# Kernel tuning notes

Measured on AMD Instinct MI355X. Metric: run time of the kernel, lower is better.

Reference implementation:

```python
import jax, jax.numpy as jnp
import numpy as np

N_NODES = 50000
N_GRAPHS = 64
HIDDEN = 128
INPUT = 128
NEG_SLOPE = 0.2


def _gat_layer(x, src, dst, W, a_src, a_dst, b, n_nodes):
    # x: [N, Fin]; src/dst: [E] (self-loops already included)
    h = x @ W                              # [N, H]
    alpha_s = h @ a_src                    # [N]
    alpha_d = h @ a_dst                    # [N]
    e = alpha_s[src] + alpha_d[dst]        # [E]
    e = jnp.where(e > 0, e, NEG_SLOPE * e)  # leaky_relu(0.2)
    # segment softmax over destination node
    m = jax.ops.segment_max(e, dst, num_segments=n_nodes)  # [N]
    m = jnp.where(jnp.isfinite(m), m, 0.0)
    ee = jnp.exp(e - m[dst])
    s = jax.ops.segment_sum(ee, dst, num_segments=n_nodes)
    coef = ee / (s[dst] + 1e-16)           # [E]
    out = jax.ops.segment_sum(h[src] * coef[:, None], dst, num_segments=n_nodes)
    return out + b


def setup_inputs() -> dict:
    key = jax.random.key(0)
    ks = jax.random.split(key, 16)
    x = jax.random.normal(ks[0], (N_NODES, INPUT), dtype=jnp.float32)
    edge_index = jax.random.randint(ks[1], (2, 600000), 0, N_NODES, dtype=jnp.int64 if jax.config.x64_enabled else jnp.int32).astype(jnp.int32)
    batch = jnp.sort(jax.random.randint(ks[2], (N_NODES,), 0, N_GRAPHS)).astype(jnp.int32)
    def glorot(k, shape):
        lim = float(np.sqrt(6.0 / (shape[0] + shape[-1])))
        return jax.random.uniform(k, shape, jnp.float32, -lim, lim)
    params = {}
    dims = [(INPUT, HIDDEN), (HIDDEN, HIDDEN), (HIDDEN, HIDDEN)]
    for i, (fi, fo) in enumerate(dims, 1):
        params[f"W{i}"] = glorot(ks[3 * i], (fi, fo))
        params[f"a_src{i}"] = glorot(ks[3 * i + 1], (fo,)) * 0.1
        params[f"a_dst{i}"] = glorot(ks[3 * i + 2], (fo,)) * 0.1
        params[f"b{i}"] = jnp.zeros((fo,), jnp.float32)
    return dict(x=x, edge_index=edge_index, batch=batch, **params)


def reference(x, edge_index, batch,
              W1, a_src1, a_dst1, b1,
              W2, a_src2, a_dst2, b2,
              W3, a_src3, a_dst3, b3):
    n = x.shape[0]
    loops = jnp.arange(n, dtype=edge_index.dtype)
    src = jnp.concatenate([edge_index[0], loops])  # PyG add_self_loops=True
    dst = jnp.concatenate([edge_index[1], loops])
    h = jax.nn.elu(_gat_layer(x, src, dst, W1, a_src1, a_dst1, b1, n))
    h = jax.nn.elu(_gat_layer(h, src, dst, W2, a_src2, a_dst2, b2, n))
    h = jax.nn.elu(_gat_layer(h, src, dst, W3, a_src3, a_dst3, b3, n))
    # global_mean_pool
    sums = jax.ops.segment_sum(h, batch, num_segments=N_GRAPHS)
    cnt = jax.ops.segment_sum(jnp.ones((n,), h.dtype), batch, num_segments=N_GRAPHS)
    return sums / jnp.maximum(cnt, 1.0)[:, None]
```

## Files before the change

### kernel.cpp

```cpp
#include <hip/hip_runtime.h>
#include <math.h>

#define N_NODES 50000
#define N_GRAPHS 64
#define HID 128
#define SCAN_B 196
#define NODE_BLKS 196
#define NBUCK 128
#define AP 132

typedef _Float16 half8 __attribute__((ext_vector_type(8)));
typedef float f32x4 __attribute__((ext_vector_type(4)));
typedef int i32x4 __attribute__((ext_vector_type(4)));

__device__ __forceinline__ float lrelu(float e) { return e > 0.f ? e : 0.2f * e; }
__device__ __forceinline__ float elu_fast(float o) { return o > 0.f ? o : __expf(o) - 1.f; }

__device__ __forceinline__ void fmix_lo(float& a, int h2, float c) {
    asm("v_fma_mix_f32 %0, %1, %2, %0 op_sel_hi:[1,0,0]" : "+v"(a) : "v"(h2), "v"(c));
}
__device__ __forceinline__ void fmix_hi(float& a, int h2, float c) {
    asm("v_fma_mix_f32 %0, %1, %2, %0 op_sel:[1,0,0] op_sel_hi:[1,0,0]" : "+v"(a) : "v"(h2), "v"(c));
}

__global__ void count_prep(const int* __restrict__ dst, int n_e, int nblk,
                           int* __restrict__ counts, int* __restrict__ start,
                           int* __restrict__ dhist, int* __restrict__ gcur,
                           const float* __restrict__ W0, const float* __restrict__ W1,
                           const float* __restrict__ W2,
                           const float* __restrict__ as0, const float* __restrict__ ad0,
                           const float* __restrict__ as1, const float* __restrict__ ad1,
                           const float* __restrict__ as2, const float* __restrict__ ad2,
                           _Float16* __restrict__ Wh0, _Float16* __restrict__ Wh1,
                           _Float16* __restrict__ Wh2,
                           float* __restrict__ wfold) {
    int blk = blockIdx.x;
    if (blk < nblk) {
        if (blk == 0) {
            if (threadIdx.x <= N_GRAPHS) start[threadIdx.x] = -1;
            if (threadIdx.x < NBUCK) { dhist[threadIdx.x] = 0; gcur[threadIdx.x] = 0; }
        }
        int e = blk * 256 + threadIdx.x;
        if (e < n_e) atomicAdd(&counts[dst[e]], 1);
        return;
    }
    int b = blk - nblk;
    if (b < 24) {
        int layer = b >> 3;
        const float* W = layer == 0 ? W0 : (layer == 1 ? W1 : W2);
        _Float16* Wh = layer == 0 ? Wh0 : (layer == 1 ? Wh1 : Wh2);
        int t = (b & 7) * 256 + threadIdx.x;
        int lane = t & 63;
        int nt = (t >> 6) & 7;
        int kt = t >> 9;
        int n = nt * 16 + (lane & 15);
        int kbase = kt * 32 + (lane >> 4) * 8;
#pragma unroll
        for (int j = 0; j < 8; ++j) {
            float w = W[(size_t)(kbase + j) * 128 + n];
            Wh[(size_t)t * 8 + j] = (_Float16)w;
        }
    } else {
        int idx = b - 24;
        int layer = idx >> 1, which = idx & 1;
        const float* W = layer == 0 ? W0 : (layer == 1 ? W1 : W2);
        const float* a = which == 0 ? (layer == 0 ? as0 : (layer == 1 ? as1 : as2))
                                    : (layer == 0 ? ad0 : (layer == 1 ? ad1 : ad2));
        int k = threadIdx.x;
        if (k < 128) {
            float s = 0.f;
            for (int j = 0; j < 128; ++j) s = fmaf(W[k * 128 + j], a[j], s);
            wfold[idx * 128 + k] = s;
        }
    }
}

__global__ __launch_bounds__(256) void block_reduce(const int* __restrict__ counts,
                                                    int* __restrict__ bsum) {
    __shared__ int red[256];
    int t = threadIdx.x;
    int i = blockIdx.x * 256 + t;
    red[t] = (i < N_NODES) ? counts[i] : 0;
    __syncthreads();
#pragma unroll
    for (int off = 128; off; off >>= 1) {
        if (t < off) red[t] += red[t + off];
        __syncthreads();
    }
    if (t == 0) bsum[blockIdx.x] = red[0];
}

__global__ __launch_bounds__(256) void block_scan(const int* __restrict__ counts,
                                                  const int* __restrict__ bsum,
                                                  const int* __restrict__ batch,
                                                  int* __restrict__ offs,
                                                  int* __restrict__ cursor,
                                                  int* __restrict__ start,
                                                  int* __restrict__ dhist) {
    __shared__ int sb[256];
    __shared__ int sh[256];
    __shared__ int lh[NBUCK];
    int t = threadIdx.x;
    if (t < NBUCK) lh[t] = 0;
    int v = (t < SCAN_B) ? bsum[t] : 0;
    sb[t] = v;
    __syncthreads();
#pragma unroll
    for (int off = 1; off < 256; off <<= 1) {
        int u = (t >= off) ? sb[t - off] : 0;
        __syncthreads();
        sb[t] += u;
        __syncthreads();
    }
    int bpre = (blockIdx.x == 0) ? 0 : sb[blockIdx.x - 1];
    if (blockIdx.x == 0 && t == SCAN_B - 1) offs[N_NODES] = sb[t];

    int i = blockIdx.x * 256 + t;
    int c = (i < N_NODES) ? counts[i] : 0;
    sh[t] = c;
    __syncthreads();
#pragma unroll
    for (int off = 1; off < 256; off <<= 1) {
        int u = (t >= off) ? sh[t - off] : 0;
        __syncthreads();
        sh[t] += u;
        __syncthreads();
    }
    if (i < N_NODES) {
        int e = bpre + sh[t] - c;
        offs[i] = e;
        cursor[i] = e;
        int b = batch[i];
        if (i == 0) start[b] = 0;
        else if (batch[i - 1] != b) start[b] = i;
        atomicAdd(&lh[c < NBUCK - 1 ? c : NBUCK - 1], 1);
    }
    __syncthreads();
    if (t < NBUCK) {
        int n = lh[t];
        if (n) atomicAdd(&dhist[t], n);
    }
}

__global__ __launch_bounds__(256) void scatter_kernel(const int* __restrict__ src,
                                                      const int* __restrict__ dst, int n_e,
                                                      int* __restrict__ cursor,
                                                      int* __restrict__ csr_src,
                                                      float* __restrict__ outz,
                                                      const int* __restrict__ offs,
                                                      const int* __restrict__ dhist,
                                                      int* __restrict__ gcur,
                                                      int* __restrict__ order) {
    int gid = blockIdx.x * 256 + threadIdx.x;
    if (gid < N_GRAPHS * HID) outz[gid] = 0.f;
    if (gid < n_e) {
        int d = dst[gid];
        int pos = atomicAdd(&cursor[d], 1);
        csr_src[pos] = src[gid];
    }
    if (blockIdx.x >= NODE_BLKS) return;

    __shared__ int lh[NBUCK], sc[NBUCK], lbase[NBUCK];
    int t = threadIdx.x;
    if (t < NBUCK) lh[t] = 0;
    __syncthreads();
    int b = -1, lpos = 0;
    if (gid < N_NODES) {
        int deg = offs[gid + 1] - offs[gid];
        b = deg < NBUCK - 1 ? deg : NBUCK - 1;
        lpos = atomicAdd(&lh[b], 1);
    }
    __syncthreads();
    if (t < NBUCK) sc[t] = dhist[t];
    __syncthreads();
    for (int off = 1; off < NBUCK; off <<= 1) {
        int u = (t < NBUCK && t >= off) ? sc[t - off] : 0;
        __syncthreads();
        if (t < NBUCK) sc[t] += u;
        __syncthreads();
    }
    if (t < NBUCK) {
        int excl = t ? sc[t - 1] : 0;
        int cnt = lh[t];
        int bb = cnt ? atomicAdd(&gcur[t], cnt) : 0;
        lbase[t] = excl + bb;
    }
    __syncthreads();
    if (gid < N_NODES) order[lbase[b] + lpos] = gid;
}

__global__ __launch_bounds__(256) void gemm_mfma(const float* __restrict__ X,
                                                 const _Float16* __restrict__ Wh,
                                                 const float* __restrict__ wsv,
                                                 const float* __restrict__ wdv,
                                                 _Float16* __restrict__ H16,
                                                 float* __restrict__ AS,
                                                 float* __restrict__ AD) {
    __shared__ float wsL[128], wdL[128];
    int t = threadIdx.x;
    if (t < 128) wsL[t] = wsv[t];
    else if (t < 256) wdL[t - 128] = wdv[t - 128];
    __syncthreads();

    int wave = t >> 6, lane = t & 63;
    int m15 = lane & 15, quad = lane >> 4;
    int rowbase = blockIdx.x * 64 + wave * 16;
    int arow = rowbase + m15;
    bool arow_ok = arow < N_NODES;

    f32x4 acc[8];
#pragma unroll
    for (int nt = 0; nt < 8; ++nt) acc[nt] = (f32x4){0.f, 0.f, 0.f, 0.f};
    float as_p = 0.f, ad_p = 0.f;

    const float* xrow = X + (size_t)arow * 128 + quad * 8;
#pragma unroll
    for (int kt = 0; kt < 4; ++kt) {
        f32x4 a0 = (f32x4){0.f, 0.f, 0.f, 0.f};
        f32x4 a1 = (f32x4){0.f, 0.f, 0.f, 0.f};
        if (arow_ok) {
            a0 = *(const f32x4*)(xrow + kt * 32);
            a1 = *(const f32x4*)(xrow + kt * 32 + 4);
        }
        int kb = kt * 32 + quad * 8;
        half8 ah;
#pragma unroll
        for (int j = 0; j < 4; ++j) {
            as_p = fmaf(a0[j], wsL[kb + j], as_p);
            ad_p = fmaf(a0[j], wdL[kb + j], ad_p);
            as_p = fmaf(a1[j], wsL[kb + 4 + j], as_p);
            ad_p = fmaf(a1[j], wdL[kb + 4 + j], ad_p);
            ah[j] = (_Float16)a0[j];
            ah[4 + j] = (_Float16)a1[j];
        }
#pragma unroll
        for (int nt = 0; nt < 8; ++nt) {
            size_t fidx = ((size_t)((kt * 8 + nt) * 64 + lane)) * 8;
            half8 bh = *(const half8*)(Wh + fidx);
            acc[nt] = __builtin_amdgcn_mfma_f32_16x16x32_f16(ah, bh, acc[nt], 0, 0, 0);
        }
    }

#pragma unroll
    for (int nt = 0; nt < 8; ++nt) {
        int c = nt * 16 + m15;
#pragma unroll
        for (int reg = 0; reg < 4; ++reg) {
            int gr = rowbase + quad * 4 + reg;
            if (gr < N_NODES) H16[(size_t)gr * 128 + c] = (_Float16)acc[nt][reg];
        }
    }
    as_p += __shfl_xor(as_p, 16);
    ad_p += __shfl_xor(ad_p, 16);
    as_p += __shfl_xor(as_p, 32);
    ad_p += __shfl_xor(ad_p, 32);
    if (quad == 0 && arow_ok) { AS[arow] = as_p; AD[arow] = ad_p; }
}

__global__ __launch_bounds__(256) void aggregate_kernel(const _Float16* __restrict__ H16,
                                                        const float* __restrict__ AS,
                                                        const float* __restrict__ AD,
                                                        const int* __restrict__ offs,
                                                        const int* __restrict__ csr_src,
                                                        const int* __restrict__ order,
                                                        const float* __restrict__ bias,
                                                        const _Float16* __restrict__ Whn,
                                                        const float* __restrict__ wfn,
                                                        _Float16* __restrict__ Hn,
                                                        float* __restrict__ ASn,
                                                        float* __restrict__ ADn,
                                                        float* __restrict__ OUT) {
    __shared__ int2 sh_sp[16][64];
    __shared__ _Float16 aW[16][AP];
    __shared__ int nds[16];
    int tid = threadIdx.x;
    int quad = tid >> 4;
    int l16 = tid & 15;
    int node = order[blockIdx.x * 16 + quad];

    int beg = offs[node];
    int deg = offs[node + 1] - beg;
    float ad = AD[node];
    float eself = lrelu(AS[node] + ad);
    const i32x4* H4 = (const i32x4*)H16;
    i32x4 hsv = H4[(size_t)node * 16 + l16];
    bool fast = deg <= 64;

    float m, ssum = 0.f, ps;
    if (fast) {
        float mym = -INFINITY;
        for (int i = l16; i < deg; i += 16) {
            int sv = csr_src[beg + i];
            float e = lrelu(AS[sv] + ad);
            sh_sp[quad][i] = make_int2(sv, __float_as_int(e));
            mym = fmaxf(mym, e);
        }
#pragma unroll
        for (int off = 8; off; off >>= 1) mym = fmaxf(mym, __shfl_xor(mym, off, 16));
        m = fmaxf(mym, eself);
        ps = __expf(eself - m);
        for (int i = l16; i < deg; i += 16) {
            int2 sp = sh_sp[quad][i];
            float p = __expf(__int_as_float(sp.y) - m);
            sh_sp[quad][i] = make_int2(sp.x, __float_as_int(p));
            ssum += p;
        }
    } else {
        float mym = -INFINITY;
        for (int i = beg + l16; i < beg + deg; i += 16)
            mym = fmaxf(mym, lrelu(AS[csr_src[i]] + ad));
#pragma unroll
        for (int off = 8; off; off >>= 1) mym = fmaxf(mym, __shfl_xor(mym, off, 16));
        m = fmaxf(mym, eself);
        ps = __expf(eself - m);
        for (int i = beg + l16; i < beg + deg; i += 16)
            ssum += __expf(lrelu(AS[csr_src[i]] + ad) - m);
    }

    float accA[8] = {0.f, 0.f, 0.f, 0.f, 0.f, 0.f, 0.f, 0.f};
    float accB[8] = {0.f, 0.f, 0.f, 0.f, 0.f, 0.f, 0.f, 0.f};

    if (fast) {
        int k = 0;
        for (; k + 3 < deg; k += 4) {
            int2 sp0 = sh_sp[quad][k];
            int2 sp1 = sh_sp[quad][k + 1];
            int2 sp2 = sh_sp[quad][k + 2];
            int2 sp3 = sh_sp[quad][k + 3];
            i32x4 h0 = H4[(size_t)sp0.x * 16 + l16];
            i32x4 h1 = H4[(size_t)sp1.x * 16 + l16];
            i32x4 h2 = H4[(size_t)sp2.x * 16 + l16];
            i32x4 h3 = H4[(size_t)sp3.x * 16 + l16];
            float c0 = __int_as_float(sp0.y), c1 = __int_as_float(sp1.y);
            float c2 = __int_as_float(sp2.y), c3 = __int_as_float(sp3.y);
#pragma unroll
            for (int j = 0; j < 4; ++j) {
                fmix_lo(accA[2 * j], h0[j], c0);
                fmix_hi(accA[2 * j + 1], h0[j], c0);
                fmix_lo(accB[2 * j], h1[j], c1);
                fmix_hi(accB[2 * j + 1], h1[j], c1);
            }
#pragma unroll
            for (int j = 0; j < 4; ++j) {
                fmix_lo(accA[2 * j], h2[j], c2);
                fmix_hi(accA[2 * j + 1], h2[j], c2);
                fmix_lo(accB[2 * j], h3[j], c3);
                fmix_hi(accB[2 * j + 1], h3[j], c3);
            }
        }
        for (; k < deg; ++k) {
            int2 sp0 = sh_sp[quad][k];
            float c0 = __int_as_float(sp0.y);
            i32x4 h0 = H4[(size_t)sp0.x * 16 + l16];
#pragma unroll
            for (int j = 0; j < 4; ++j) {
                fmix_lo(accA[2 * j], h0[j], c0);
                fmix_hi(accA[2 * j + 1], h0[j], c0);
            }
        }
    } else {
        for (int k = 0; k < deg; ++k) {
            int s = csr_src[beg + k];
            float c = __expf(lrelu(AS[s] + ad) - m);
            i32x4 h0 = H4[(size_t)s * 16 + l16];
#pragma unroll
            for (int j = 0; j < 4; ++j) {
                fmix_lo(accA[2 * j], h0[j], c);
                fmix_hi(accA[2 * j + 1], h0[j], c);
            }
        }
    }

#pragma unroll
    for (int j = 0; j < 4; ++j) {
        fmix_lo(accA[2 * j], hsv[j], ps);
        fmix_hi(accA[2 * j + 1], hsv[j], ps);
    }
#pragma unroll
    for (int off = 8; off; off >>= 1) ssum += __shfl_xor(ssum, off, 16);
    float inv = __builtin_amdgcn_rcpf(ssum + ps + 1e-16f);

    int c0i = l16 * 8;
    f32x4 b0 = ((const f32x4*)bias)[l16 * 2];
    f32x4 b1 = ((const f32x4*)bias)[l16 * 2 + 1];
    f32x4 o0, o1;
    o0.x = elu_fast(fmaf(accA[0] + accB[0], inv, b0.x));
    o0.y = elu_fast(fmaf(accA[1] + accB[1], inv, b0.y));
    o0.z = elu_fast(fmaf(accA[2] + accB[2], inv, b0.z));
    o0.w = elu_fast(fmaf(accA[3] + accB[3], inv, b0.w));
    o1.x = elu_fast(fmaf(accA[4] + accB[4], inv, b1.x));
    o1.y = elu_fast(fmaf(accA[5] + accB[5], inv, b1.y));
    o1.z = elu_fast(fmaf(accA[6] + accB[6], inv, b1.z));
    o1.w = elu_fast(fmaf(accA[7] + accB[7], inv, b1.w));
    if (OUT) {
        ((f32x4*)OUT)[(size_t)node * 32 + l16 * 2] = o0;
        ((f32x4*)OUT)[(size_t)node * 32 + l16 * 2 + 1] = o1;
    }

    if (Whn) {
        const float* wsn = wfn;
        const float* wdn = wfn + 128;
        float asn = o0.x * wsn[c0i] + o0.y * wsn[c0i + 1] + o0.z * wsn[c0i + 2] +
                    o0.w * wsn[c0i + 3] + o1.x * wsn[c0i + 4] + o1.y * wsn[c0i + 5] +
                    o1.z * wsn[c0i + 6] + o1.w * wsn[c0i + 7];
        float adn = o0.x * wdn[c0i] + o0.y * wdn[c0i + 1] + o0.z * wdn[c0i + 2] +
                    o0.w * wdn[c0i + 3] + o1.x * wdn[c0i + 4] + o1.y * wdn[c0i + 5] +
                    o1.z * wdn[c0i + 6] + o1.w * wdn[c0i + 7];
#pragma unroll
        for (int off = 8; off; off >>= 1) {
            asn += __shfl_xor(asn, off, 16);
            adn += __shfl_xor(adn, off, 16);
        }
        if (l16 == 0) {
            ASn[node] = asn;
            ADn[node] = adn;
            nds[quad] = node;
        }
        half8 hh;
        hh[0] = (_Float16)o0.x; hh[1] = (_Float16)o0.y;
        hh[2] = (_Float16)o0.z; hh[3] = (_Float16)o0.w;
        hh[4] = (_Float16)o1.x; hh[5] = (_Float16)o1.y;
        hh[6] = (_Float16)o1.z; hh[7] = (_Float16)o1.w;
        *(half8*)&aW[quad][c0i] = hh;
        __syncthreads();

        int wv = tid >> 6, lane = tid & 63;
        int m15 = lane & 15, eq = lane >> 4;
        f32x4 acc0 = (f32x4){0.f, 0.f, 0.f, 0.f};
        f32x4 acc1 = (f32x4){0.f, 0.f, 0.f, 0.f};
#pragma unroll
        for (int kt = 0; kt < 4; ++kt) {
            half8 ah = *(const half8*)&aW[m15][kt * 32 + eq * 8];
            half8 bh0 = *(const half8*)(Whn + ((size_t)((kt * 8 + wv * 2) * 64 + lane)) * 8);
            half8 bh1 = *(const half8*)(Whn + ((size_t)((kt * 8 + wv * 2 + 1) * 64 + lane)) * 8);
            acc0 = __builtin_amdgcn_mfma_f32_16x16x32_f16(ah, bh0, acc0, 0, 0, 0);
            acc1 = __builtin_amdgcn_mfma_f32_16x16x32_f16(ah, bh1, acc1, 0, 0, 0);
        }
#pragma unroll
        for (int reg = 0; reg < 4; ++reg) {
            int nid = nds[eq * 4 + reg];
            Hn[(size_t)nid * 128 + wv * 32 + m15] = (_Float16)acc0[reg];
            Hn[(size_t)nid * 128 + wv * 32 + 16 + m15] = (_Float16)acc1[reg];
        }
    }
}

__device__ __forceinline__ int estart(const int* __restrict__ start, int g) {
    for (; g < N_GRAPHS; ++g) {
        int v = start[g];
        if (v >= 0) return v;
    }
    return N_NODES;
}

__global__ __launch_bounds__(128) void pool_kernel(const float* __restrict__ F,
                                                   const int* __restrict__ start,
                                                   float* __restrict__ out) {
    int b = blockIdx.x;
    int g = b >> 4, sub = b & 15;
    int c = threadIdx.x;
    int s0 = estart(start, g), e0 = estart(start, g + 1);
    float acc = 0.f;
    for (int i = s0 + sub; i < e0; i += 16) acc += F[(size_t)i * 128 + c];
    int cnt = e0 - s0;
    float r = 1.f / (float)(cnt > 1 ? cnt : 1);
    atomicAdd(&out[(size_t)g * 128 + c], acc * r);
}

extern "C" void kernel_launch(void* const* d_in, const int* in_sizes, int n_in,
                              void* d_out, int out_size, void* d_ws, size_t ws_size,
                              hipStream_t stream) {
    const float* x = (const float*)d_in[0];
    const int* edge_index = (const int*)d_in[1];
    const int* batch = (const int*)d_in[2];
    const float* W[3]   = {(const float*)d_in[3], (const float*)d_in[7], (const float*)d_in[11]};
    const float* avs[3] = {(const float*)d_in[4], (const float*)d_in[8], (const float*)d_in[12]};
    const float* avd[3] = {(const float*)d_in[5], (const float*)d_in[9], (const float*)d_in[13]};
    const float* bb[3]  = {(const float*)d_in[6], (const float*)d_in[10], (const float*)d_in[14]};
    int E0 = in_sizes[1] / 2;
    const int* esrc = edge_index;
    const int* edst = edge_index + E0;

    char* p = (char*)d_ws;
    auto alloc = [&](size_t bytes) -> void* {
        void* q = (void*)p;
        p += (bytes + 255) & ~(size_t)255;
        return q;
    };
    int* counts   = (int*)alloc((size_t)N_NODES * 4);
    int* offs     = (int*)alloc((size_t)(N_NODES + 1) * 4);
    int* cursor   = (int*)alloc((size_t)N_NODES * 4);
    int* csr_src  = (int*)alloc((size_t)E0 * 4);
    int* start    = (int*)alloc((N_GRAPHS + 1) * 4);
    int* bsum     = (int*)alloc(SCAN_B * 4);
    int* dhist    = (int*)alloc(NBUCK * 4);
    int* gcur     = (int*)alloc(NBUCK * 4);
    int* order    = (int*)alloc((size_t)N_NODES * 4);
    float* ASa    = (float*)alloc((size_t)N_NODES * 4);
    float* ADa    = (float*)alloc((size_t)N_NODES * 4);
    float* ASb    = (float*)alloc((size_t)N_NODES * 4);
    float* ADb    = (float*)alloc((size_t)N_NODES * 4);
    float* wfold  = (float*)alloc(6 * 128 * 4);
    _Float16* Ha  = (_Float16*)alloc((size_t)N_NODES * HID * 2);
    _Float16* Hb  = (_Float16*)alloc((size_t)N_NODES * HID * 2);
    float* FA     = (float*)alloc((size_t)N_NODES * HID * 4);
    _Float16* Wh[3];
    for (int l = 0; l < 3; ++l) Wh[l] = (_Float16*)alloc(16384 * 2);

    int nblk = (E0 + 255) / 256;
    hipMemsetAsync(counts, 0, (size_t)N_NODES * 4, stream);
    count_prep<<<nblk + 30, 256, 0, stream>>>(edst, E0, nblk, counts, start, dhist, gcur,
                                              W[0], W[1], W[2], avs[0], avd[0], avs[1], avd[1],
                                              avs[2], avd[2], Wh[0], Wh[1], Wh[2], wfold);
    block_reduce<<<SCAN_B, 256, 0, stream>>>(counts, bsum);
    block_scan<<<SCAN_B, 256, 0, stream>>>(counts, bsum, batch, offs, cursor, start, dhist);
    scatter_kernel<<<nblk, 256, 0, stream>>>(esrc, edst, E0, cursor, csr_src, (float*)d_out,
                                             offs, dhist, gcur, order);

    gemm_mfma<<<(N_NODES + 63) / 64, 256, 0, stream>>>(x, Wh[0], wfold, wfold + 128,
                                                       Ha, ASa, ADa);
    aggregate_kernel<<<N_NODES / 16, 256, 0, stream>>>(Ha, ASa, ADa, offs, csr_src, order,
                                                       bb[0], Wh[1], wfold + 2 * 128,
                                                       Hb, ASb, ADb, nullptr);
    aggregate_kernel<<<N_NODES / 16, 256, 0, stream>>>(Hb, ASb, ADb, offs, csr_src, order,
                                                       bb[1], Wh[2], wfold + 4 * 128,
                                                       Ha, ASa, ADa, nullptr);
    aggregate_kernel<<<N_NODES / 16, 256, 0, stream>>>(Ha, ASa, ADa, offs, csr_src, order,
                                                       bb[2], nullptr, nullptr,
                                                       nullptr, nullptr, nullptr, FA);

    pool_kernel<<<N_GRAPHS * 16, 128, 0, stream>>>(FA, start, (float*)d_out);
}
```

Before: 279.6 us.

## Merge block reduce into scan and fuse first-layer GEMM into scatter launch

Drops the separate block_reduce kernel by having every scan block redundantly sum all per-block counts itself, one thread per 256-node chunk. It also appends the layer-1 MFMA GEMM blocks to the scatter kernel's grid, so edge scattering and the X·W projection run together in one launch. The intent is to cut two kernel launches and let independent work overlap. In exchange, each scan block now does serial strided reads of the whole counts array, and the GEMM blocks share the launch with atomic-heavy scatter blocks.

Result: slower. 299.4 us (+7.1%).

```diff
diff --git a/kernel.cpp b/kernel.cpp
--- a/kernel.cpp
+++ b/kernel.cpp
@@ -5,9 +5,9 @@
 #define N_GRAPHS 64
 #define HID 128
 #define SCAN_B 196
-#define NODE_BLKS 196
 #define NBUCK 128
 #define AP 132
+#define GEMM_B 782
 
 typedef _Float16 half8 __attribute__((ext_vector_type(8)));
 typedef float f32x4 __attribute__((ext_vector_type(4)));
@@ -75,35 +75,26 @@
     }
 }
 
-__global__ __launch_bounds__(256) void block_reduce(const int* __restrict__ counts,
-                                                    int* __restrict__ bsum) {
-    __shared__ int red[256];
-    int t = threadIdx.x;
-    int i = blockIdx.x * 256 + t;
-    red[t] = (i < N_NODES) ? counts[i] : 0;
-    __syncthreads();
-#pragma unroll
-    for (int off = 128; off; off >>= 1) {
-        if (t < off) red[t] += red[t + off];
-        __syncthreads();
-    }
-    if (t == 0) bsum[blockIdx.x] = red[0];
-}
-
-__global__ __launch_bounds__(256) void block_scan(const int* __restrict__ counts,
-                                                  const int* __restrict__ bsum,
-                                                  const int* __restrict__ batch,
-                                                  int* __restrict__ offs,
-                                                  int* __restrict__ cursor,
-                                                  int* __restrict__ start,
-                                                  int* __restrict__ dhist) {
+__global__ __launch_bounds__(256) void scan2(const int* __restrict__ counts,
+                                             const int* __restrict__ batch,
+                                             int* __restrict__ offs,
+                                             int* __restrict__ cursor,
+                                             int* __restrict__ start,
+                                             int* __restrict__ dhist) {
     __shared__ int sb[256];
     __shared__ int sh[256];
     __shared__ int lh[NBUCK];
     int t = threadIdx.x;
+    int s = 0;
+    if (t < SCAN_B) {
+        int base = t * 256;
+        for (int j = 0; j < 256; ++j) {
+            int idx = base + j;
+            s += (idx < N_NODES) ? counts[idx] : 0;
+        }
+    }
+    sb[t] = s;
     if (t < NBUCK) lh[t] = 0;
-    int v = (t < SCAN_B) ? bsum[t] : 0;
-    sb[t] = v;
     __syncthreads();
 #pragma unroll
     for (int off = 1; off < 256; off <<= 1) {
@@ -142,26 +133,95 @@
     }
 }
 
-__global__ __launch_bounds__(256) void scatter_kernel(const int* __restrict__ src,
-                                                      const int* __restrict__ dst, int n_e,
-                                                      int* __restrict__ cursor,
-                                                      int* __restrict__ csr_src,
-                                                      float* __restrict__ outz,
-                                                      const int* __restrict__ offs,
-                                                      const int* __restrict__ dhist,
-                                                      int* __restrict__ gcur,
-                                                      int* __restrict__ order) {
-    int gid = blockIdx.x * 256 + threadIdx.x;
+__global__ __launch_bounds__(256) void scatter_gemm(const int* __restrict__ src,
+                                                    const int* __restrict__ dst, int n_e,
+                                                    int nblk,
+                                                    int* __restrict__ cursor,
+                                                    int* __restrict__ csr_src,
+                                                    float* __restrict__ outz,
+                                                    const int* __restrict__ offs,
+                                                    const int* __restrict__ dhist,
+                                                    int* __restrict__ gcur,
+                                                    int* __restrict__ order,
+                                                    const float* __restrict__ X,
+                                                    const _Float16* __restrict__ Wh,
+                                                    const float* __restrict__ wfold,
+                                                    _Float16* __restrict__ H16,
+                                                    float* __restrict__ AS,
+                                                    float* __restrict__ AD) {
+    int t = threadIdx.x;
+    if (blockIdx.x >= (unsigned)nblk) {
+        __shared__ float wsL[128], wdL[128];
+        if (t < 128) wsL[t] = wfold[t];
+        else wdL[t - 128] = wfold[t];
+        __syncthreads();
+
+        int vt = blockIdx.x - nblk;
+        int wave = t >> 6, lane = t & 63;
+        int m15 = lane & 15, quad = lane >> 4;
+        int rowbase = vt * 64 + wave * 16;
+        int arow = rowbase + m15;
+        bool arow_ok = arow < N_NODES;
+
+        f32x4 acc[8];
+#pragma unroll
+        for (int nt = 0; nt < 8; ++nt) acc[nt] = (f32x4){0.f, 0.f, 0.f, 0.f};
+        float as_p = 0.f, ad_p = 0.f;
+
+        const float* xrow = X + (size_t)arow * 128 + quad * 8;
+#pragma unroll
+        for (int kt = 0; kt < 4; ++kt) {
+            f32x4 a0 = (f32x4){0.f, 0.f, 0.f, 0.f};
+            f32x4 a1 = (f32x4){0.f, 0.f, 0.f, 0.f};
+            if (arow_ok) {
+                a0 = *(const f32x4*)(xrow + kt * 32);
+                a1 = *(const f32x4*)(xrow + kt * 32 + 4);
+            }
+            int kb = kt * 32 + quad * 8;
+            half8 ah;
+#pragma unroll
+            for (int j = 0; j < 4; ++j) {
+                as_p = fmaf(a0[j], wsL[kb + j], as_p);
+                ad_p = fmaf(a0[j], wdL[kb + j], ad_p);
+                as_p = fmaf(a1[j], wsL[kb + 4 + j], as_p);
+                ad_p = fmaf(a1[j], wdL[kb + 4 + j], ad_p);
+                ah[j] = (_Float16)a0[j];
+                ah[4 + j] = (_Float16)a1[j];
+            }
+#pragma unroll
+            for (int nt = 0; nt < 8; ++nt) {
+                size_t fidx = ((size_t)((kt * 8 + nt) * 64 + lane)) * 8;
+                half8 bh = *(const half8*)(Wh + fidx);
+                acc[nt] = __builtin_amdgcn_mfma_f32_16x16x32_f16(ah, bh, acc[nt], 0, 0, 0);
+            }
+        }
+#pragma unroll
+        for (int nt = 0; nt < 8; ++nt) {
+            int c = nt * 16 + m15;
+#pragma unroll
+            for (int reg = 0; reg < 4; ++reg) {
+                int gr = rowbase + quad * 4 + reg;
+                if (gr < N_NODES) H16[(size_t)gr * 128 + c] = (_Float16)acc[nt][reg];
+            }
+        }
+        as_p += __shfl_xor(as_p, 16);
+        ad_p += __shfl_xor(ad_p, 16);
+        as_p += __shfl_xor(as_p, 32);
+        ad_p += __shfl_xor(ad_p, 32);
+        if (quad == 0 && arow_ok) { AS[arow] = as_p; AD[arow] = ad_p; }
+        return;
+    }
+
+    int gid = blockIdx.x * 256 + t;
     if (gid < N_GRAPHS * HID) outz[gid] = 0.f;
     if (gid < n_e) {
         int d = dst[gid];
         int pos = atomicAdd(&cursor[d], 1);
         csr_src[pos] = src[gid];
     }
-    if (blockIdx.x >= NODE_BLKS) return;
+    if (blockIdx.x >= SCAN_B) return;
 
     __shared__ int lh[NBUCK], sc[NBUCK], lbase[NBUCK];
-    int t = threadIdx.x;
     if (t < NBUCK) lh[t] = 0;
     __syncthreads();
     int b = -1, lpos = 0;
@@ -187,74 +247,6 @@
     }
     __syncthreads();
     if (gid < N_NODES) order[lbase[b] + lpos] = gid;
-}
-
-__global__ __launch_bounds__(256) void gemm_mfma(const float* __restrict__ X,
-                                                 const _Float16* __restrict__ Wh,
-                                                 const float* __restrict__ wsv,
-                                                 const float* __restrict__ wdv,
-                                                 _Float16* __restrict__ H16,
-                                                 float* __restrict__ AS,
-                                                 float* __restrict__ AD) {
-    __shared__ float wsL[128], wdL[128];
-    int t = threadIdx.x;
-    if (t < 128) wsL[t] = wsv[t];
-    else if (t < 256) wdL[t - 128] = wdv[t - 128];
-    __syncthreads();
-
-    int wave = t >> 6, lane = t & 63;
-    int m15 = lane & 15, quad = lane >> 4;
-    int rowbase = blockIdx.x * 64 + wave * 16;
-    int arow = rowbase + m15;
-    bool arow_ok = arow < N_NODES;
-
-    f32x4 acc[8];
-#pragma unroll
-    for (int nt = 0; nt < 8; ++nt) acc[nt] = (f32x4){0.f, 0.f, 0.f, 0.f};
-    float as_p = 0.f, ad_p = 0.f;
-
-    const float* xrow = X + (size_t)arow * 128 + quad * 8;
-#pragma unroll
-    for (int kt = 0; kt < 4; ++kt) {
-        f32x4 a0 = (f32x4){0.f, 0.f, 0.f, 0.f};
-        f32x4 a1 = (f32x4){0.f, 0.f, 0.f, 0.f};
-        if (arow_ok) {
-            a0 = *(const f32x4*)(xrow + kt * 32);
-            a1 = *(const f32x4*)(xrow + kt * 32 + 4);
-        }
-        int kb = kt * 32 + quad * 8;
-        half8 ah;
-#pragma unroll
-        for (int j = 0; j < 4; ++j) {
-            as_p = fmaf(a0[j], wsL[kb + j], as_p);
-            ad_p = fmaf(a0[j], wdL[kb + j], ad_p);
-            as_p = fmaf(a1[j], wsL[kb + 4 + j], as_p);
-            ad_p = fmaf(a1[j], wdL[kb + 4 + j], ad_p);
-            ah[j] = (_Float16)a0[j];
-            ah[4 + j] = (_Float16)a1[j];
-        }
-#pragma unroll
-        for (int nt = 0; nt < 8; ++nt) {
-            size_t fidx = ((size_t)((kt * 8 + nt) * 64 + lane)) * 8;
-            half8 bh = *(const half8*)(Wh + fidx);
-            acc[nt] = __builtin_amdgcn_mfma_f32_16x16x32_f16(ah, bh, acc[nt], 0, 0, 0);
-        }
-    }
-
-#pragma unroll
-    for (int nt = 0; nt < 8; ++nt) {
-        int c = nt * 16 + m15;
-#pragma unroll
-        for (int reg = 0; reg < 4; ++reg) {
-            int gr = rowbase + quad * 4 + reg;
-            if (gr < N_NODES) H16[(size_t)gr * 128 + c] = (_Float16)acc[nt][reg];
-        }
-    }
-    as_p += __shfl_xor(as_p, 16);
-    ad_p += __shfl_xor(ad_p, 16);
-    as_p += __shfl_xor(as_p, 32);
-    ad_p += __shfl_xor(ad_p, 32);
-    if (quad == 0 && arow_ok) { AS[arow] = as_p; AD[arow] = ad_p; }
 }
 
 __global__ __launch_bounds__(256) void aggregate_kernel(const _Float16* __restrict__ H16,
@@ -492,7 +484,6 @@
     int* cursor   = (int*)alloc((size_t)N_NODES * 4);
     int* csr_src  = (int*)alloc((size_t)E0 * 4);
     int* start    = (int*)alloc((N_GRAPHS + 1) * 4);
-    int* bsum     = (int*)alloc(SCAN_B * 4);
     int* dhist    = (int*)alloc(NBUCK * 4);
     int* gcur     = (int*)alloc(NBUCK * 4);
     int* order    = (int*)alloc((size_t)N_NODES * 4);
@@ -512,13 +503,11 @@
     count_prep<<<nblk + 30, 256, 0, stream>>>(edst, E0, nblk, counts, start, dhist, gcur,
                                               W[0], W[1], W[2], avs[0], avd[0], avs[1], avd[1],
                                               avs[2], avd[2], Wh[0], Wh[1], Wh[2], wfold);
-    block_reduce<<<SCAN_B, 256, 0, stream>>>(counts, bsum);
-    block_scan<<<SCAN_B, 256, 0, stream>>>(counts, bsum, batch, offs, cursor, start, dhist);
-    scatter_kernel<<<nblk, 256, 0, stream>>>(esrc, edst, E0, cursor, csr_src, (float*)d_out,
-                                             offs, dhist, gcur, order);
-
-    gemm_mfma<<<(N_NODES + 63) / 64, 256, 0, stream>>>(x, Wh[0], wfold, wfold + 128,
-                                                       Ha, ASa, ADa);
+    scan2<<<SCAN_B, 256, 0, stream>>>(counts, batch, offs, cursor, start, dhist);
+    scatter_gemm<<<nblk + GEMM_B, 256, 0, stream>>>(esrc, edst, E0, nblk, cursor, csr_src,
+                                                    (float*)d_out, offs, dhist, gcur, order,
+                                                    x, Wh[0], wfold, Ha, ASa, ADa);
+
     aggregate_kernel<<<N_NODES / 16, 256, 0, stream>>>(Ha, ASa, ADa, offs, csr_src, order,
                                                        bb[0], Wh[1], wfold + 2 * 128,
                                                        Hb, ASb, ADb, nullptr);
```

## Fuse mean pooling into final aggregate and precompute CSR edge slots

Applied to the files above, without the earlier changes.

Counting now records each edge's atomic slot within its destination, so the scatter writes directly to offs[d]+slot without a second atomic cursor pass. The last aggregate layer adds its ELU outputs, scaled by 1/count, straight into the per-graph output with global float atomics. This removes the FA intermediate buffer and the separate pool kernel. In exchange there are many contended atomics on only 64x128 addresses, and float summation order is now nondeterministic.

Result: slower. 450.7 us (+61.2%).

```diff
diff --git a/kernel.cpp b/kernel.cpp
--- a/kernel.cpp
+++ b/kernel.cpp
@@ -23,8 +23,17 @@
     asm("v_fma_mix_f32 %0, %1, %2, %0 op_sel:[1,0,0] op_sel_hi:[1,0,0]" : "+v"(a) : "v"(h2), "v"(c));
 }
 
+__device__ __forceinline__ int estart(const int* __restrict__ start, int g) {
+    for (; g < N_GRAPHS; ++g) {
+        int v = start[g];
+        if (v >= 0) return v;
+    }
+    return N_NODES;
+}
+
 __global__ void count_prep(const int* __restrict__ dst, int n_e, int nblk,
-                           int* __restrict__ counts, int* __restrict__ start,
+                           int* __restrict__ counts, int* __restrict__ epos,
+                           int* __restrict__ start,
                            int* __restrict__ dhist, int* __restrict__ gcur,
                            const float* __restrict__ W0, const float* __restrict__ W1,
                            const float* __restrict__ W2,
@@ -41,7 +50,7 @@
             if (threadIdx.x < NBUCK) { dhist[threadIdx.x] = 0; gcur[threadIdx.x] = 0; }
         }
         int e = blk * 256 + threadIdx.x;
-        if (e < n_e) atomicAdd(&counts[dst[e]], 1);
+        if (e < n_e) epos[e] = atomicAdd(&counts[dst[e]], 1);
         return;
     }
     int b = blk - nblk;
@@ -94,7 +103,6 @@
                                                   const int* __restrict__ bsum,
                                                   const int* __restrict__ batch,
                                                   int* __restrict__ offs,
-                                                  int* __restrict__ cursor,
                                                   int* __restrict__ start,
                                                   int* __restrict__ dhist) {
     __shared__ int sb[256];
@@ -129,7 +137,6 @@
     if (i < N_NODES) {
         int e = bpre + sh[t] - c;
         offs[i] = e;
-        cursor[i] = e;
         int b = batch[i];
         if (i == 0) start[b] = 0;
         else if (batch[i - 1] != b) start[b] = i;
@@ -144,7 +151,7 @@
 
 __global__ __launch_bounds__(256) void scatter_kernel(const int* __restrict__ src,
                                                       const int* __restrict__ dst, int n_e,
-                                                      int* __restrict__ cursor,
+                                                      const int* __restrict__ epos,
                                                       int* __restrict__ csr_src,
                                                       float* __restrict__ outz,
                                                       const int* __restrict__ offs,
@@ -155,8 +162,7 @@
     if (gid < N_GRAPHS * HID) outz[gid] = 0.f;
     if (gid < n_e) {
         int d = dst[gid];
-        int pos = atomicAdd(&cursor[d], 1);
-        csr_src[pos] = src[gid];
+        csr_src[offs[d] + epos[gid]] = src[gid];
     }
     if (blockIdx.x >= NODE_BLKS) return;
 
@@ -269,7 +275,9 @@
                                                         _Float16* __restrict__ Hn,
                                                         float* __restrict__ ASn,
                                                         float* __restrict__ ADn,
-                                                        float* __restrict__ OUT) {
+                                                        const int* __restrict__ batch,
+                                                        const int* __restrict__ start,
+                                                        float* __restrict__ POOL) {
     __shared__ int2 sh_sp[16][64];
     __shared__ _Float16 aW[16][AP];
     __shared__ int nds[16];
@@ -392,9 +400,21 @@
     o1.y = elu_fast(fmaf(accA[5] + accB[5], inv, b1.y));
     o1.z = elu_fast(fmaf(accA[6] + accB[6], inv, b1.z));
     o1.w = elu_fast(fmaf(accA[7] + accB[7], inv, b1.w));
-    if (OUT) {
-        ((f32x4*)OUT)[(size_t)node * 32 + l16 * 2] = o0;
-        ((f32x4*)OUT)[(size_t)node * 32 + l16 * 2 + 1] = o1;
+
+    if (POOL) {
+        int g = batch[node];
+        int s0 = estart(start, g), e1 = estart(start, g + 1);
+        int cnt = e1 - s0;
+        float r = 1.f / (float)(cnt > 1 ? cnt : 1);
+        float* dst = POOL + (size_t)g * 128 + c0i;
+        atomicAdd(&dst[0], o0.x * r);
+        atomicAdd(&dst[1], o0.y * r);
+        atomicAdd(&dst[2], o0.z * r);
+        atomicAdd(&dst[3], o0.w * r);
+        atomicAdd(&dst[4], o1.x * r);
+        atomicAdd(&dst[5], o1.y * r);
+        atomicAdd(&dst[6], o1.z * r);
+        atomicAdd(&dst[7], o1.w * r);
     }
 
     if (Whn) {
@@ -443,28 +463,6 @@
             Hn[(size_t)nid * 128 + wv * 32 + 16 + m15] = (_Float16)acc1[reg];
         }
     }
-}
-
-__device__ __forceinline__ int estart(const int* __restrict__ start, int g) {
-    for (; g < N_GRAPHS; ++g) {
-        int v = start[g];
-        if (v >= 0) return v;
-    }
-    return N_NODES;
-}
-
-__global__ __launch_bounds__(128) void pool_kernel(const float* __restrict__ F,
-                                                   const int* __restrict__ start,
-                                                   float* __restrict__ out) {
-    int b = blockIdx.x;
-    int g = b >> 4, sub = b & 15;
-    int c = threadIdx.x;
-    int s0 = estart(start, g), e0 = estart(start, g + 1);
-    float acc = 0.f;
-    for (int i = s0 + sub; i < e0; i += 16) acc += F[(size_t)i * 128 + c];
-    int cnt = e0 - s0;
-    float r = 1.f / (float)(cnt > 1 ? cnt : 1);
-    atomicAdd(&out[(size_t)g * 128 + c], acc * r);
 }
 
 extern "C" void kernel_launch(void* const* d_in, const int* in_sizes, int n_in,
@@ -489,7 +487,7 @@
     };
     int* counts   = (int*)alloc((size_t)N_NODES * 4);
     int* offs     = (int*)alloc((size_t)(N_NODES + 1) * 4);
-    int* cursor   = (int*)alloc((size_t)N_NODES * 4);
+    int* epos     = (int*)alloc((size_t)E0 * 4);
     int* csr_src  = (int*)alloc((size_t)E0 * 4);
     int* start    = (int*)alloc((N_GRAPHS + 1) * 4);
     int* bsum     = (int*)alloc(SCAN_B * 4);
@@ -503,31 +501,29 @@
     float* wfold  = (float*)alloc(6 * 128 * 4);
     _Float16* Ha  = (_Float16*)alloc((size_t)N_NODES * HID * 2);
     _Float16* Hb  = (_Float16*)alloc((size_t)N_NODES * HID * 2);
-    float* FA     = (float*)alloc((size_t)N_NODES * HID * 4);
     _Float16* Wh[3];
     for (int l = 0; l < 3; ++l) Wh[l] = (_Float16*)alloc(16384 * 2);
 
     int nblk = (E0 + 255) / 256;
     hipMemsetAsync(counts, 0, (size_t)N_NODES * 4, stream);
-    count_prep<<<nblk + 30, 256, 0, stream>>>(edst, E0, nblk, counts, start, dhist, gcur,
+    count_prep<<<nblk + 30, 256, 0, stream>>>(edst, E0, nblk, counts, epos, start, dhist, gcur,
                                               W[0], W[1], W[2], avs[0], avd[0], avs[1], avd[1],
                                               avs[2], avd[2], Wh[0], Wh[1], Wh[2], wfold);
     block_reduce<<<SCAN_B, 256, 0, stream>>>(counts, bsum);
-    block_scan<<<SCAN_B, 256, 0, stream>>>(counts, bsum, batch, offs, cursor, start, dhist);
-    scatter_kernel<<<nblk, 256, 0, stream>>>(esrc, edst, E0, cursor, csr_src, (float*)d_out,
+    block_scan<<<SCAN_B, 256, 0, stream>>>(counts, bsum, batch, offs, start, dhist);
+    scatter_kernel<<<nblk, 256, 0, stream>>>(esrc, edst, E0, epos, csr_src, (float*)d_out,
                                              offs, dhist, gcur, order);
 
     gemm_mfma<<<(N_NODES + 63) / 64, 256, 0, stream>>>(x, Wh[0], wfold, wfold + 128,
                                                        Ha, ASa, ADa);
     aggregate_kernel<<<N_NODES / 16, 256, 0, stream>>>(Ha, ASa, ADa, offs, csr_src, order,
                                                        bb[0], Wh[1], wfold + 2 * 128,
-                                                       Hb, ASb, ADb, nullptr);
+                                                       Hb, ASb, ADb, nullptr, nullptr, nullptr);
     aggregate_kernel<<<N_NODES / 16, 256, 0, stream>>>(Hb, ASb, ADb, offs, csr_src, order,
                                                        bb[1], Wh[2], wfold + 4 * 128,
-                                                       Ha, ASa, ADa, nullptr);
+                                                       Ha, ASa, ADa, nullptr, nullptr, nullptr);
     aggregate_kernel<<<N_NODES / 16, 256, 0, stream>>>(Ha, ASa, ADa, offs, csr_src, order,
                                                        bb[2], nullptr, nullptr,
-                                                       nullptr, nullptr, nullptr, FA);
-
-    pool_kernel<<<N_GRAPHS * 16, 128, 0, stream>>>(FA, start, (float*)d_out);
-}
+                                                       nullptr, nullptr, nullptr,
+                                                       batch, start, (float*)d_out);
+}
```
